# Kernel tuning notes

Hardware: AMD Instinct MI355X
Metric: run time of the kernel (lower is better)

## Reference

```python
import jax, jax.numpy as jnp
import numpy as np
from jax.scipy.special import ndtr, ndtri

B, N, K = 64, 4096, 128
MU, SIGMA = 0.0, 1.0
_TINY = 1e-7


def setup_inputs() -> dict:
    key = jax.random.key(0)
    k1, k2, k3 = jax.random.split(key, 3)
    C = jax.random.randint(k1, (B, N), 0, K)                      # labels [B,N]
    eps = jax.random.normal(k2, (B, N), dtype=jnp.float32)        # std-normal noise for upper bounds
    U = jax.random.uniform(k3, (B, N, K), dtype=jnp.float32)      # uniforms for inverse-CDF truncnorm
    return {
        "C": C,
        "eps": eps,
        "U": U,
        "mu": jnp.full((1,), MU, dtype=jnp.float32),
        "sigma": jnp.full((1,), SIGMA, dtype=jnp.float32),
    }


def reference(C, eps, U, mu, sigma):
    # Relabel ground-truth labels to 0..K-1 (torch.unique(..., return_inverse=True))
    _, C_new = jnp.unique(C, return_inverse=True)
    C_new = C_new.reshape(C.shape)                                # [B,N]
    Kdim = U.shape[-1]
    # upper bound per (b,i): u ~ N(mu, sigma), reparameterized
    u = mu.reshape(()) + sigma.reshape(()) * eps                  # [B,N]
    # truncnorm.rvs(-inf, u) via inverse CDF: z = Phi^{-1}(U * Phi(u))
    Uc = jnp.clip(U, _TINY, 1.0 - _TINY)
    Z = ndtri(Uc * ndtr(u)[..., None])                            # [B,N,K]
    # Z[b,i,C_new[b,i]] = u[b,i]
    onehot = C_new[..., None] == jnp.arange(Kdim)                 # [B,N,K] bool
    return jnp.where(onehot, u[..., None], Z)
```

## Files before the change

kernel.cpp:

```cpp
#include <hip/hip_runtime.h>
#include <math.h>


__device__ __forceinline__ float ndtri_acklam(float p) {
    const float omp = 1.0f - p;
    const bool upper = p > 0.5f;
    const float pm = upper ? omp : p;
    float x;
    if (pm < 0.02425f) {
        float q = sqrtf(-2.0f * __logf(pm));
        float num = -0.007784894002430293f;
        num = fmaf(num, q, -0.3223964580411365f);
        num = fmaf(num, q, -2.400758277161838f);
        num = fmaf(num, q, -2.549732539343734f);
        num = fmaf(num, q,  4.374664141464968f);
        num = fmaf(num, q,  2.938163982698783f);
        float den = 0.007784695709041462f;
        den = fmaf(den, q, 0.3224671290700398f);
        den = fmaf(den, q, 2.445134137142996f);
        den = fmaf(den, q, 3.754408661907416f);
        den = fmaf(den, q, 1.0f);
        x = num * __builtin_amdgcn_rcpf(den);
        if (upper) x = -x;
    } else {
        float q = p - 0.5f;
        float r = q * q;
        float num = -39.69683028665376f;
        num = fmaf(num, r,  220.9460984245205f);
        num = fmaf(num, r, -275.9285104469687f);
        num = fmaf(num, r,  138.3577518672690f);
        num = fmaf(num, r,  -30.66479806614716f);
        num = fmaf(num, r,    2.506628277459239f);
        float den = -54.47609879822406f;
        den = fmaf(den, r,  161.5858368580409f);
        den = fmaf(den, r, -155.6989798598866f);
        den = fmaf(den, r,   66.80131188771972f);
        den = fmaf(den, r,  -13.28068155288572f);
        den = fmaf(den, r,    1.0f);
        x = q * num * __builtin_amdgcn_rcpf(den);
    }
    return x;
}

__global__ void __launch_bounds__(256) row_kernel(
    const int* __restrict__ C,
    const float* __restrict__ eps,
    const float* __restrict__ mu_p,
    const float* __restrict__ sigma_p,
    unsigned* __restrict__ mask,
    float2* __restrict__ uphi,
    int n)
{
    __shared__ unsigned sm[4];
    if (threadIdx.x < 4) sm[threadIdx.x] = 0u;
    __syncthreads();

    int i = blockIdx.x * blockDim.x + threadIdx.x;
    unsigned m0 = 0, m1 = 0, m2 = 0, m3 = 0;
    if (i < n) {
        int c = C[i];
        float u = fmaf(sigma_p[0], eps[i], mu_p[0]);
        float phi = 0.5f * erfcf(-u * 0.7071067811865476f);
        uphi[i] = make_float2(u, phi);
        unsigned bit = 1u << (c & 31);
        int w = (c >> 5) & 3;
        m0 = (w == 0) ? bit : 0u;
        m1 = (w == 1) ? bit : 0u;
        m2 = (w == 2) ? bit : 0u;
        m3 = (w == 3) ? bit : 0u;
    }
    #pragma unroll
    for (int off = 32; off > 0; off >>= 1) {
        m0 |= __shfl_down(m0, off, 64);
        m1 |= __shfl_down(m1, off, 64);
        m2 |= __shfl_down(m2, off, 64);
        m3 |= __shfl_down(m3, off, 64);
    }
    if ((threadIdx.x & 63) == 0) {
        if (m0) atomicOr(&sm[0], m0);
        if (m1) atomicOr(&sm[1], m1);
        if (m2) atomicOr(&sm[2], m2);
        if (m3) atomicOr(&sm[3], m3);
    }
    __syncthreads();
    if (threadIdx.x < 4) {
        unsigned v = sm[threadIdx.x];
        if (v) atomicOr(&mask[threadIdx.x], v);
    }
}

__global__ void __launch_bounds__(256) map_kernel(
    const int* __restrict__ C,
    const float4* __restrict__ U4,
    const float2* __restrict__ uphi,
    const unsigned* __restrict__ mask,
    float4* __restrict__ out4,
    int total4)
{
    int idx = blockIdx.x * blockDim.x + threadIdx.x;
    if (idx >= total4) return;
    int row = idx >> 5;
    int k0  = (idx & 31) << 2;

    float2 up = uphi[row];
    float u = up.x;
    float phi = up.y;

    int c = C[row];
    unsigned w0 = mask[0], w1 = mask[1], w2 = mask[2], w3 = mask[3];
    int cw = c >> 5;
    unsigned below = (1u << (c & 31)) - 1u;
    int rank = __popc(w0 & ((0 < cw) ? 0xFFFFFFFFu : ((0 == cw) ? below : 0u)))
             + __popc(w1 & ((1 < cw) ? 0xFFFFFFFFu : ((1 == cw) ? below : 0u)))
             + __popc(w2 & ((2 < cw) ? 0xFFFFFFFFu : ((2 == cw) ? below : 0u)))
             + __popc(w3 & ((3 < cw) ? 0xFFFFFFFFu : ((3 == cw) ? below : 0u)));

    float4 Uv = U4[idx];
    const float lo = 1e-7f;
    const float hi = 0.99999988079071045f;

    float p0 = fminf(fmaxf(Uv.x, lo), hi) * phi;
    float p1 = fminf(fmaxf(Uv.y, lo), hi) * phi;
    float p2 = fminf(fmaxf(Uv.z, lo), hi) * phi;
    float p3 = fminf(fmaxf(Uv.w, lo), hi) * phi;

    float z0 = ndtri_acklam(p0);
    float z1 = ndtri_acklam(p1);
    float z2 = ndtri_acklam(p2);
    float z3 = ndtri_acklam(p3);

    float4 o;
    o.x = (k0 + 0 == rank) ? u : z0;
    o.y = (k0 + 1 == rank) ? u : z1;
    o.z = (k0 + 2 == rank) ? u : z2;
    o.w = (k0 + 3 == rank) ? u : z3;
    out4[idx] = o;
}

extern "C" void kernel_launch(void* const* d_in, const int* in_sizes, int n_in,
                              void* d_out, int out_size, void* d_ws, size_t ws_size,
                              hipStream_t stream) {
    const int*   C     = (const int*)d_in[0];
    const float* eps   = (const float*)d_in[1];
    const float4* U4   = (const float4*)d_in[2];
    const float* mu    = (const float*)d_in[3];
    const float* sigma = (const float*)d_in[4];
    float4* out4 = (float4*)d_out;

    unsigned* mask = (unsigned*)d_ws;
    float2* uphi = (float2*)((char*)d_ws + 256);

    int n = in_sizes[0];
    int total4 = out_size / 4;

    hipMemsetAsync(d_ws, 0, 4 * sizeof(unsigned), stream);

    int rb = (n + 255) / 256;
    row_kernel<<<rb, 256, 0, stream>>>(C, eps, mu, sigma, mask, uphi, n);

    int mb = (total4 + 255) / 256;
    map_kernel<<<mb, 256, 0, stream>>>(C, U4, uphi, mask, out4, total4);
}
```

Before: 245.8 us.

## Vectorize row kernel, branchless ndtri, nontemporal stores, med3 clamp

Several unrelated tweaks land together. The row kernel now handles four rows per thread with int4/float4 loads. ndtri evaluates both the tail and central polynomial branches and picks one by select, which removes divergence but does more arithmetic per element. The map kernel reads the mask as a single uint4, clamps with fmed3, and writes the output with nontemporal stores to reduce cache pollution on the large write stream. The kernel is mostly memory-bound, so the extra ALU work from the branchless ndtri could offset the gains.

Result: no change. 242.7 us (-1.3%).

```diff
diff --git a/kernel.cpp b/kernel.cpp
--- a/kernel.cpp
+++ b/kernel.cpp
@@ -2,44 +2,56 @@
 #include <math.h>
 
 
-__device__ __forceinline__ float ndtri_acklam(float p) {
-    const float omp = 1.0f - p;
+typedef float vfloat4 __attribute__((ext_vector_type(4)));
+
+__device__ __forceinline__ float ndtri_fast(float p) {
+    const float omp  = 1.0f - p;
     const bool upper = p > 0.5f;
-    const float pm = upper ? omp : p;
-    float x;
-    if (pm < 0.02425f) {
-        float q = sqrtf(-2.0f * __logf(pm));
-        float num = -0.007784894002430293f;
-        num = fmaf(num, q, -0.3223964580411365f);
-        num = fmaf(num, q, -2.400758277161838f);
-        num = fmaf(num, q, -2.549732539343734f);
-        num = fmaf(num, q,  4.374664141464968f);
-        num = fmaf(num, q,  2.938163982698783f);
-        float den = 0.007784695709041462f;
-        den = fmaf(den, q, 0.3224671290700398f);
-        den = fmaf(den, q, 2.445134137142996f);
-        den = fmaf(den, q, 3.754408661907416f);
-        den = fmaf(den, q, 1.0f);
-        x = num * __builtin_amdgcn_rcpf(den);
-        if (upper) x = -x;
-    } else {
-        float q = p - 0.5f;
-        float r = q * q;
-        float num = -39.69683028665376f;
-        num = fmaf(num, r,  220.9460984245205f);
-        num = fmaf(num, r, -275.9285104469687f);
-        num = fmaf(num, r,  138.3577518672690f);
-        num = fmaf(num, r,  -30.66479806614716f);
-        num = fmaf(num, r,    2.506628277459239f);
-        float den = -54.47609879822406f;
-        den = fmaf(den, r,  161.5858368580409f);
-        den = fmaf(den, r, -155.6989798598866f);
-        den = fmaf(den, r,   66.80131188771972f);
-        den = fmaf(den, r,  -13.28068155288572f);
-        den = fmaf(den, r,    1.0f);
-        x = q * num * __builtin_amdgcn_rcpf(den);
-    }
-    return x;
+    const float pm   = upper ? omp : p;
+    const bool tail  = pm < 0.02425f;
+
+    float qt = sqrtf(-2.0f * __logf(pm));
+    float numT = -0.007784894002430293f;
+    numT = fmaf(numT, qt, -0.3223964580411365f);
+    numT = fmaf(numT, qt, -2.400758277161838f);
+    numT = fmaf(numT, qt, -2.549732539343734f);
+    numT = fmaf(numT, qt,  4.374664141464968f);
+    numT = fmaf(numT, qt,  2.938163982698783f);
+    float denT = 0.007784695709041462f;
+    denT = fmaf(denT, qt, 0.3224671290700398f);
+    denT = fmaf(denT, qt, 2.445134137142996f);
+    denT = fmaf(denT, qt, 3.754408661907416f);
+    denT = fmaf(denT, qt, 1.0f);
+
+    float qc = p - 0.5f;
+    float r  = qc * qc;
+    float numC = -39.69683028665376f;
+    numC = fmaf(numC, r,  220.9460984245205f);
+    numC = fmaf(numC, r, -275.9285104469687f);
+    numC = fmaf(numC, r,  138.3577518672690f);
+    numC = fmaf(numC, r,  -30.66479806614716f);
+    numC = fmaf(numC, r,    2.506628277459239f);
+    float denC = -54.47609879822406f;
+    denC = fmaf(denC, r,  161.5858368580409f);
+    denC = fmaf(denC, r, -155.6989798598866f);
+    denC = fmaf(denC, r,   66.80131188771972f);
+    denC = fmaf(denC, r,  -13.28068155288572f);
+    denC = fmaf(denC, r,    1.0f);
+
+    float num = tail ? numT : numC;
+    float den = tail ? denT : denC;
+    float s   = tail ? (upper ? -1.0f : 1.0f) : qc;
+    return s * num * __builtin_amdgcn_rcpf(den);
+}
+
+__device__ __forceinline__ void set_label_bit(int c, unsigned& m0, unsigned& m1,
+                                              unsigned& m2, unsigned& m3) {
+    unsigned bit = 1u << (c & 31);
+    int w = (c >> 5) & 3;
+    if      (w == 0) m0 |= bit;
+    else if (w == 1) m1 |= bit;
+    else if (w == 2) m2 |= bit;
+    else             m3 |= bit;
 }
 
 __global__ void __launch_bounds__(256) row_kernel(
@@ -55,20 +67,43 @@
     if (threadIdx.x < 4) sm[threadIdx.x] = 0u;
     __syncthreads();
 
+    const float sg = sigma_p[0];
+    const float mu = mu_p[0];
+    const float kInvSqrt2 = 0.7071067811865476f;
+
     int i = blockIdx.x * blockDim.x + threadIdx.x;
+    int base = i << 2;
     unsigned m0 = 0, m1 = 0, m2 = 0, m3 = 0;
-    if (i < n) {
-        int c = C[i];
-        float u = fmaf(sigma_p[0], eps[i], mu_p[0]);
-        float phi = 0.5f * erfcf(-u * 0.7071067811865476f);
-        uphi[i] = make_float2(u, phi);
-        unsigned bit = 1u << (c & 31);
-        int w = (c >> 5) & 3;
-        m0 = (w == 0) ? bit : 0u;
-        m1 = (w == 1) ? bit : 0u;
-        m2 = (w == 2) ? bit : 0u;
-        m3 = (w == 3) ? bit : 0u;
-    }
+
+    if (base + 3 < n) {
+        int4   c = *reinterpret_cast<const int4*>(C + base);
+        float4 e = *reinterpret_cast<const float4*>(eps + base);
+        float u0 = fmaf(sg, e.x, mu);
+        float u1 = fmaf(sg, e.y, mu);
+        float u2 = fmaf(sg, e.z, mu);
+        float u3 = fmaf(sg, e.w, mu);
+        float p0 = 0.5f * erfcf(-u0 * kInvSqrt2);
+        float p1 = 0.5f * erfcf(-u1 * kInvSqrt2);
+        float p2 = 0.5f * erfcf(-u2 * kInvSqrt2);
+        float p3 = 0.5f * erfcf(-u3 * kInvSqrt2);
+        float4* op = reinterpret_cast<float4*>(uphi + base);
+        op[0] = make_float4(u0, p0, u1, p1);
+        op[1] = make_float4(u2, p2, u3, p3);
+        set_label_bit(c.x, m0, m1, m2, m3);
+        set_label_bit(c.y, m0, m1, m2, m3);
+        set_label_bit(c.z, m0, m1, m2, m3);
+        set_label_bit(c.w, m0, m1, m2, m3);
+    } else if (base < n) {
+        for (int j = 0; j < 4 && base + j < n; ++j) {
+            int cc = C[base + j];
+            float ee = eps[base + j];
+            float uu = fmaf(sg, ee, mu);
+            float pp = 0.5f * erfcf(-uu * kInvSqrt2);
+            uphi[base + j] = make_float2(uu, pp);
+            set_label_bit(cc, m0, m1, m2, m3);
+        }
+    }
+
     #pragma unroll
     for (int off = 32; off > 0; off >>= 1) {
         m0 |= __shfl_down(m0, off, 64);
@@ -93,7 +128,7 @@
     const int* __restrict__ C,
     const float4* __restrict__ U4,
     const float2* __restrict__ uphi,
-    const unsigned* __restrict__ mask,
+    const uint4* __restrict__ mask4,
     float4* __restrict__ out4,
     int total4)
 {
@@ -102,39 +137,41 @@
     int row = idx >> 5;
     int k0  = (idx & 31) << 2;
 
+    float4 Uv = U4[idx];
     float2 up = uphi[row];
+    int c = C[row];
+    uint4 w = *mask4;
+
+    int cw = c >> 5;
+    unsigned below = (1u << (c & 31)) - 1u;
+    int rank = __popc(w.x & ((0 < cw) ? 0xFFFFFFFFu : ((0 == cw) ? below : 0u)))
+             + __popc(w.y & ((1 < cw) ? 0xFFFFFFFFu : ((1 == cw) ? below : 0u)))
+             + __popc(w.z & ((2 < cw) ? 0xFFFFFFFFu : ((2 == cw) ? below : 0u)))
+             + __popc(w.w & ((3 < cw) ? 0xFFFFFFFFu : ((3 == cw) ? below : 0u)));
+
     float u = up.x;
     float phi = up.y;
 
-    int c = C[row];
-    unsigned w0 = mask[0], w1 = mask[1], w2 = mask[2], w3 = mask[3];
-    int cw = c >> 5;
-    unsigned below = (1u << (c & 31)) - 1u;
-    int rank = __popc(w0 & ((0 < cw) ? 0xFFFFFFFFu : ((0 == cw) ? below : 0u)))
-             + __popc(w1 & ((1 < cw) ? 0xFFFFFFFFu : ((1 == cw) ? below : 0u)))
-             + __popc(w2 & ((2 < cw) ? 0xFFFFFFFFu : ((2 == cw) ? below : 0u)))
-             + __popc(w3 & ((3 < cw) ? 0xFFFFFFFFu : ((3 == cw) ? below : 0u)));
-
-    float4 Uv = U4[idx];
     const float lo = 1e-7f;
     const float hi = 0.99999988079071045f;
 
-    float p0 = fminf(fmaxf(Uv.x, lo), hi) * phi;
-    float p1 = fminf(fmaxf(Uv.y, lo), hi) * phi;
-    float p2 = fminf(fmaxf(Uv.z, lo), hi) * phi;
-    float p3 = fminf(fmaxf(Uv.w, lo), hi) * phi;
-
-    float z0 = ndtri_acklam(p0);
-    float z1 = ndtri_acklam(p1);
-    float z2 = ndtri_acklam(p2);
-    float z3 = ndtri_acklam(p3);
-
-    float4 o;
+    float p0 = __builtin_amdgcn_fmed3f(Uv.x, lo, hi) * phi;
+    float p1 = __builtin_amdgcn_fmed3f(Uv.y, lo, hi) * phi;
+    float p2 = __builtin_amdgcn_fmed3f(Uv.z, lo, hi) * phi;
+    float p3 = __builtin_amdgcn_fmed3f(Uv.w, lo, hi) * phi;
+
+    float z0 = ndtri_fast(p0);
+    float z1 = ndtri_fast(p1);
+    float z2 = ndtri_fast(p2);
+    float z3 = ndtri_fast(p3);
+
+    vfloat4 o;
     o.x = (k0 + 0 == rank) ? u : z0;
     o.y = (k0 + 1 == rank) ? u : z1;
     o.z = (k0 + 2 == rank) ? u : z2;
     o.w = (k0 + 3 == rank) ? u : z3;
-    out4[idx] = o;
+
+    __builtin_nontemporal_store(o, reinterpret_cast<vfloat4*>(&out4[idx]));
 }
 
 extern "C" void kernel_launch(void* const* d_in, const int* in_sizes, int n_in,
@@ -153,11 +190,12 @@
     int n = in_sizes[0];
     int total4 = out_size / 4;
 
-    hipMemsetAsync(d_ws, 0, 4 * sizeof(unsigned), stream);
-
-    int rb = (n + 255) / 256;
+    (void)hipMemsetAsync(d_ws, 0, 4 * sizeof(unsigned), stream);
+
+    int n4 = (n + 3) >> 2;
+    int rb = (n4 + 255) / 256;
     row_kernel<<<rb, 256, 0, stream>>>(C, eps, mu, sigma, mask, uphi, n);
 
     int mb = (total4 + 255) / 256;
-    map_kernel<<<mb, 256, 0, stream>>>(C, U4, uphi, mask, out4, total4);
-}
+    map_kernel<<<mb, 256, 0, stream>>>(C, U4, uphi, (const uint4*)mask, out4, total4);
+}
```
